# Optimization experiments

Measured on AMD Instinct MI355X. Metric: run time of the kernel, lower is better.

The kernel has to match this reference:

```python
import jax, jax.numpy as jnp
import numpy as np

B, N, D_MODEL, H, D_K, D_V = 4, 1024, 1024, 16, 64, 1024  # N == D_V required by the module's output matmul


def setup_inputs() -> dict:
    key = jax.random.key(0)
    ks = jax.random.split(key, 7)
    def xavier(k, shape):
        fan_in, fan_out = shape[-2], shape[-1]
        std = (2.0 / (fan_in + fan_out)) ** 0.5
        return jax.random.normal(k, shape, dtype=jnp.float32) * std
    return {
        "query": jax.random.normal(ks[0], (B, N, D_MODEL), dtype=jnp.float32),
        "key": jax.random.normal(ks[1], (B, N, D_MODEL), dtype=jnp.float32),
        "value": jax.random.normal(ks[2], (B, N, D_MODEL), dtype=jnp.float32),
        "w_q": xavier(ks[3], (H, D_MODEL, D_K)),
        "w_k": xavier(ks[4], (H, D_MODEL, D_K)),
        "w_v": xavier(ks[5], (H, D_MODEL, D_V)),
        "w_o": xavier(ks[6], (D_MODEL, H * D_V)),
    }


def reference(query, key, value, w_q, w_k, w_v, w_o):
    # Per-head projections: [B,N,d_model] x [H,d_model,d] -> [B,H,N,d]
    q = jnp.einsum('bnd,hdk->bhnk', query, w_q)
    k = jnp.einsum('bnd,hdk->bhnk', key, w_k)
    v = jnp.einsum('bnd,hdv->bhnv', value, w_v)
    scale = 1.0 / jnp.sqrt(jnp.asarray(q.shape[-1], q.dtype))
    scores = jnp.einsum('bhqk,bhmk->bhqm', q, k) * scale  # [B,H,N,N]
    weights = jax.nn.softmax(scores, axis=-1)
    out = jnp.einsum('bhqm,bhmv->bhqv', weights, v)  # [B,H,N,d_v]
    out = out.reshape(out.shape[0], -1, out.shape[-1])  # [B, H*N, d_v]
    # Faithful to source: torch.matmul(w_o, output) with w_o [d_model, H*d_v];
    # requires H*d_v == H*N (N == d_v); result [B, d_model, d_v].
    return jnp.einsum('de,bev->bdv', w_o, out)
```

## Files before the change

### kernel.cpp

```cpp
#include <hip/hip_runtime.h>
#include <hip/hip_bf16.h>

typedef __hip_bfloat16 bf16;
typedef __attribute__((ext_vector_type(8))) short short8;
typedef __attribute__((ext_vector_type(4))) float floatx4;

#define BK 64
#define LDK 72

template<bool OUT_BF16, bool A_F32, bool B_F32>
__global__ void __launch_bounds__(256) gemm_nt(
    const void* __restrict__ Av, const void* __restrict__ Bv, void* __restrict__ Cv,
    int M, int N, int K, int lda, int ldb, int ldc,
    long sA, long sB, long sC)
{
    __shared__ __align__(16) bf16 As[128 * LDK];
    __shared__ __align__(16) bf16 Bs[128 * LDK];

    int bx = blockIdx.x, by = blockIdx.y, bz = blockIdx.z;
    if (gridDim.x == 8 && gridDim.y == 8 && (gridDim.z & 7) == 0) {
        int hw  = bx + (by << 3) + (bz << 6);
        int xcd = hw & 7;
        int idx = hw >> 3;
        int zper = gridDim.z >> 3;
        bz = xcd * zper + (idx >> 6);
        int rem = idx & 63;
        by = rem >> 3;
        bx = rem & 7;
    }

    long aoff = (long)bz * sA;
    long boff = (long)bz * sB;
    long coff = (long)bz * sC;

    int m0 = by * 128;
    int n0 = bx * 128;
    int tid  = threadIdx.x;
    int lane = tid & 63;
    int wave = tid >> 6;
    int quad = lane >> 4;
    int l16  = lane & 15;
    int wm = (wave >> 1) * 64;
    int wn = (wave & 1) * 64;

    int sr = tid >> 3;
    int sc = (tid & 7) * 8;

    floatx4 acc[4][4] = {};

    uint4  pa[4], pb[4];
    float4 pa0[4], pa1[4], pb0[4], pb1[4];

    const int nt = K / BK;

#pragma unroll
    for (int s = 0; s < 4; s++) {
        int r = sr + 32 * s;
        int gm = m0 + r;
        if (A_F32) {
            const float* p = (const float*)Av + aoff + (long)gm * lda + sc;
            if (gm < M) { pa0[s] = *(const float4*)p; pa1[s] = *(const float4*)(p + 4); }
            else { pa0[s] = {0,0,0,0}; pa1[s] = {0,0,0,0}; }
        } else {
            pa[s] = (gm < M) ? *(const uint4*)((const bf16*)Av + aoff + (long)gm * lda + sc)
                             : (uint4){0,0,0,0};
        }
        int gn = n0 + r;
        if (B_F32) {
            const float* p = (const float*)Bv + boff + (long)gn * ldb + sc;
            if (gn < N) { pb0[s] = *(const float4*)p; pb1[s] = *(const float4*)(p + 4); }
            else { pb0[s] = {0,0,0,0}; pb1[s] = {0,0,0,0}; }
        } else {
            pb[s] = (gn < N) ? *(const uint4*)((const bf16*)Bv + boff + (long)gn * ldb + sc)
                             : (uint4){0,0,0,0};
        }
    }

    for (int kt = 0; kt < nt; kt++) {
        __syncthreads();
#pragma unroll
        for (int s = 0; s < 4; s++) {
            int r = sr + 32 * s;
            if (A_F32) {
                bf16 t[8];
                t[0]=__float2bfloat16(pa0[s].x); t[1]=__float2bfloat16(pa0[s].y);
                t[2]=__float2bfloat16(pa0[s].z); t[3]=__float2bfloat16(pa0[s].w);
                t[4]=__float2bfloat16(pa1[s].x); t[5]=__float2bfloat16(pa1[s].y);
                t[6]=__float2bfloat16(pa1[s].z); t[7]=__float2bfloat16(pa1[s].w);
                *(uint4*)(&As[r * LDK + sc]) = *(const uint4*)t;
            } else {
                *(uint4*)(&As[r * LDK + sc]) = pa[s];
            }
            if (B_F32) {
                bf16 t[8];
                t[0]=__float2bfloat16(pb0[s].x); t[1]=__float2bfloat16(pb0[s].y);
                t[2]=__float2bfloat16(pb0[s].z); t[3]=__float2bfloat16(pb0[s].w);
                t[4]=__float2bfloat16(pb1[s].x); t[5]=__float2bfloat16(pb1[s].y);
                t[6]=__float2bfloat16(pb1[s].z); t[7]=__float2bfloat16(pb1[s].w);
                *(uint4*)(&Bs[r * LDK + sc]) = *(const uint4*)t;
            } else {
                *(uint4*)(&Bs[r * LDK + sc]) = pb[s];
            }
        }
        __syncthreads();

        if (kt + 1 < nt) {
            int k0 = (kt + 1) * BK;
#pragma unroll
            for (int s = 0; s < 4; s++) {
                int r = sr + 32 * s;
                int gm = m0 + r;
                if (A_F32) {
                    const float* p = (const float*)Av + aoff + (long)gm * lda + k0 + sc;
                    if (gm < M) { pa0[s] = *(const float4*)p; pa1[s] = *(const float4*)(p + 4); }
                    else { pa0[s] = {0,0,0,0}; pa1[s] = {0,0,0,0}; }
                } else {
                    pa[s] = (gm < M) ? *(const uint4*)((const bf16*)Av + aoff + (long)gm * lda + k0 + sc)
                                     : (uint4){0,0,0,0};
                }
                int gn = n0 + r;
                if (B_F32) {
                    const float* p = (const float*)Bv + boff + (long)gn * ldb + k0 + sc;
                    if (gn < N) { pb0[s] = *(const float4*)p; pb1[s] = *(const float4*)(p + 4); }
                    else { pb0[s] = {0,0,0,0}; pb1[s] = {0,0,0,0}; }
                } else {
                    pb[s] = (gn < N) ? *(const uint4*)((const bf16*)Bv + boff + (long)gn * ldb + k0 + sc)
                                     : (uint4){0,0,0,0};
                }
            }
        }

#pragma unroll
        for (int ks = 0; ks < 2; ks++) {
            short8 af[4], bfr[4];
#pragma unroll
            for (int i = 0; i < 4; i++)
                af[i] = *(const short8*)(&As[(wm + i * 16 + l16) * LDK + ks * 32 + quad * 8]);
#pragma unroll
            for (int j = 0; j < 4; j++)
                bfr[j] = *(const short8*)(&Bs[(wn + j * 16 + l16) * LDK + ks * 32 + quad * 8]);
#pragma unroll
            for (int i = 0; i < 4; i++)
#pragma unroll
                for (int j = 0; j < 4; j++)
                    acc[i][j] = __builtin_amdgcn_mfma_f32_16x16x32_bf16(af[i], bfr[j], acc[i][j], 0, 0, 0);
        }
    }

#pragma unroll
    for (int i = 0; i < 4; i++) {
        int row = m0 + wm + i * 16 + quad * 4;
#pragma unroll
        for (int j = 0; j < 4; j++) {
            int col = n0 + wn + j * 16 + l16;
            if (col >= N) continue;
#pragma unroll
            for (int v = 0; v < 4; v++) {
                int r = row + v;
                if (r < M) {
                    float val = acc[i][j][v];
                    if (OUT_BF16)
                        ((bf16*)Cv)[coff + (long)r * ldc + col] = __float2bfloat16(val);
                    else
                        ((float*)Cv)[coff + (long)r * ldc + col] = val;
                }
            }
        }
    }
}

__global__ void __launch_bounds__(256) attn_softmax(
    const bf16* __restrict__ Q, const bf16* __restrict__ Kb, bf16* __restrict__ Wts)
{
    __shared__ __align__(16) bf16 Ks[64 * 72];

    int h = blockIdx.y;
    const bf16* Qbh = Q  + (long)h * 262144;
    const bf16* Kbh = Kb + (long)h * 262144;
    bf16* W = Wts + (long)h * 1048576;

    int tid  = threadIdx.x;
    int lane = tid & 63;
    int wave = tid >> 6;
    int quad = lane >> 4;
    int l16  = lane & 15;
    int q0 = blockIdx.x * 64 + wave * 16;

    short8 a0 = *(const short8*)(Qbh + (long)(q0 + l16) * 64 + quad * 8);
    short8 a1 = *(const short8*)(Qbh + (long)(q0 + l16) * 64 + 32 + quad * 8);

    int sr = tid >> 3;
    int sc = (tid & 7) * 8;

    const float scale = 0.125f;
    float m_v[4] = {-1e30f, -1e30f, -1e30f, -1e30f};
    float l_v[4] = {0.f, 0.f, 0.f, 0.f};

    for (int t = 0; t < 16; t++) {
        __syncthreads();
        const bf16* src = Kbh + (long)(t * 64 + sr) * 64 + sc;
        *(uint4*)(&Ks[sr * 72 + sc])        = *(const uint4*)src;
        *(uint4*)(&Ks[(sr + 32) * 72 + sc]) = *(const uint4*)(src + 32 * 64);
        __syncthreads();
#pragma unroll
        for (int j = 0; j < 4; j++) {
            short8 b0 = *(const short8*)(&Ks[(j * 16 + l16) * 72 + quad * 8]);
            short8 b1 = *(const short8*)(&Ks[(j * 16 + l16) * 72 + 32 + quad * 8]);
            floatx4 acc = {0.f, 0.f, 0.f, 0.f};
            acc = __builtin_amdgcn_mfma_f32_16x16x32_bf16(a0, b0, acc, 0, 0, 0);
            acc = __builtin_amdgcn_mfma_f32_16x16x32_bf16(a1, b1, acc, 0, 0, 0);
#pragma unroll
            for (int v = 0; v < 4; v++) {
                float s  = acc[v] * scale;
                float nm = fmaxf(m_v[v], s);
                l_v[v] = l_v[v] * __expf(m_v[v] - nm) + __expf(s - nm);
                m_v[v] = nm;
            }
        }
    }

#pragma unroll
    for (int d = 1; d < 16; d <<= 1) {
#pragma unroll
        for (int v = 0; v < 4; v++) {
            float om = __shfl_xor(m_v[v], d);
            float ol = __shfl_xor(l_v[v], d);
            float nm = fmaxf(m_v[v], om);
            l_v[v] = l_v[v] * __expf(m_v[v] - nm) + ol * __expf(om - nm);
            m_v[v] = nm;
        }
    }
    float linv[4];
#pragma unroll
    for (int v = 0; v < 4; v++) linv[v] = 1.0f / l_v[v];

    for (int t = 0; t < 16; t++) {
        __syncthreads();
        const bf16* src = Kbh + (long)(t * 64 + sr) * 64 + sc;
        *(uint4*)(&Ks[sr * 72 + sc])        = *(const uint4*)src;
        *(uint4*)(&Ks[(sr + 32) * 72 + sc]) = *(const uint4*)(src + 32 * 64);
        __syncthreads();
#pragma unroll
        for (int j = 0; j < 4; j++) {
            short8 b0 = *(const short8*)(&Ks[(j * 16 + l16) * 72 + quad * 8]);
            short8 b1 = *(const short8*)(&Ks[(j * 16 + l16) * 72 + 32 + quad * 8]);
            floatx4 acc = {0.f, 0.f, 0.f, 0.f};
            acc = __builtin_amdgcn_mfma_f32_16x16x32_bf16(a0, b0, acc, 0, 0, 0);
            acc = __builtin_amdgcn_mfma_f32_16x16x32_bf16(a1, b1, acc, 0, 0, 0);
#pragma unroll
            for (int v = 0; v < 4; v++) {
                float w = __expf(acc[v] * scale - m_v[v]) * linv[v];
                W[(long)(q0 + quad * 4 + v) * 1024 + t * 64 + j * 16 + l16] = __float2bfloat16(w);
            }
        }
    }
}

__global__ void __launch_bounds__(256) cast_bf16_k(
    const float* __restrict__ in, bf16* __restrict__ out, int n4)
{
    int i = blockIdx.x * 256 + threadIdx.x;
    if (i >= n4) return;
    float4 v = ((const float4*)in)[i];
    bf16 t[4] = {__float2bfloat16(v.x), __float2bfloat16(v.y),
                 __float2bfloat16(v.z), __float2bfloat16(v.w)};
    ((uint2*)out)[i] = *(const uint2*)t;
}

__global__ void __launch_bounds__(256) transpose_cast(
    const float* __restrict__ in, bf16* __restrict__ out, int R, int C)
{
    __shared__ float t[32][33];
    int h = blockIdx.z;
    const float* inh = in + (long)h * R * C;
    bf16* outh = out + (long)h * R * C;
    int c0 = blockIdx.x * 32, r0 = blockIdx.y * 32;
    int tx = threadIdx.x, ty = threadIdx.y;
#pragma unroll
    for (int i = 0; i < 32; i += 8)
        t[ty + i][tx] = inh[(long)(r0 + ty + i) * C + c0 + tx];
    __syncthreads();
#pragma unroll
    for (int i = 0; i < 32; i += 8)
        outh[(long)(c0 + ty + i) * R + r0 + tx] = __float2bfloat16(t[tx][ty + i]);
}

__global__ void __launch_bounds__(256) reduce16_k(
    const float* __restrict__ part, float* __restrict__ out)
{
    int i = blockIdx.x * 256 + threadIdx.x;
    float4 s = ((const float4*)part)[i];
#pragma unroll
    for (int c = 1; c < 16; c++) {
        float4 p = ((const float4*)part)[c * 262144 + i];
        s.x += p.x; s.y += p.y; s.z += p.z; s.w += p.w;
    }
    ((float4*)out)[i] = s;
}

extern "C" void kernel_launch(void* const* d_in, const int* in_sizes, int n_in,
                              void* d_out, int out_size, void* d_ws, size_t ws_size,
                              hipStream_t stream) {
    const float* query = (const float*)d_in[0];
    const float* key   = (const float*)d_in[1];
    const float* value = (const float*)d_in[2];
    const float* w_q   = (const float*)d_in[3];
    const float* w_k   = (const float*)d_in[4];
    const float* w_v   = (const float*)d_in[5];
    const float* w_o   = (const float*)d_in[6];
    float* out = (float*)d_out;

    char* ws = (char*)d_ws;
    const size_t MB = (size_t)1 << 20;
    bf16* wqt      = (bf16*)(ws + 0 * MB);
    bf16* wkt      = (bf16*)(ws + 2 * MB);
    bf16* wvt      = (bf16*)(ws + 4 * MB);
    bf16* wob      = (bf16*)(ws + 36 * MB);
    bf16* qb       = (bf16*)(ws + 68 * MB);
    bf16* kb       = (bf16*)(ws + 76 * MB);
    bf16* vt_b     = (bf16*)(ws + 84 * MB);
    bf16* wts_b    = (bf16*)(ws + 116 * MB);
    bf16* att_b    = (bf16*)(ws + 148 * MB);
    float* out_part = (float*)(ws + 84 * MB);

    transpose_cast<<<dim3(2, 32, 16),  dim3(32, 8), 0, stream>>>(w_q, wqt, 1024, 64);
    transpose_cast<<<dim3(2, 32, 16),  dim3(32, 8), 0, stream>>>(w_k, wkt, 1024, 64);
    transpose_cast<<<dim3(32, 32, 16), dim3(32, 8), 0, stream>>>(w_v, wvt, 1024, 1024);
    cast_bf16_k<<<16384, 256, 0, stream>>>(w_o, wob, 1024 * 16384 / 4);

    gemm_nt<true, true, false><<<dim3(1, 32, 16), 256, 0, stream>>>(
        query, wqt, qb, 4096, 64, 1024, 1024, 1024, 64, 0L, 65536L, 262144L);
    gemm_nt<true, true, false><<<dim3(1, 32, 16), 256, 0, stream>>>(
        key, wkt, kb, 4096, 64, 1024, 1024, 1024, 64, 0L, 65536L, 262144L);

    for (int b = 0; b < 4; b++) {
        gemm_nt<true, false, true><<<dim3(8, 8, 16), 256, 0, stream>>>(
            wvt, value + (long)b * 1048576, vt_b,
            1024, 1024, 1024, 1024, 1024, 1024, 1048576L, 0L, 1048576L);

        attn_softmax<<<dim3(16, 16), 256, 0, stream>>>(
            qb + (long)b * 65536, kb + (long)b * 65536, wts_b);

        gemm_nt<true, false, false><<<dim3(8, 8, 16), 256, 0, stream>>>(
            vt_b, wts_b, att_b,
            1024, 1024, 1024, 1024, 1024, 16384, 1048576L, 1048576L, 1024L);

        gemm_nt<false, false, false><<<dim3(8, 8, 16), 256, 0, stream>>>(
            wob, att_b, out_part,
            1024, 1024, 1024, 16384, 16384, 1024, 1024L, 1024L, 1048576L);

        reduce16_k<<<1024, 256, 0, stream>>>(out_part, out + (long)b * 1048576);
    }

    (void)in_sizes; (void)n_in; (void)out_size; (void)ws_size;
}
```

Measured before the change: 1.022 ms.

## Add direct global-to-LDS bf16 GEMM with XOR swizzle for the big matmuls

Adds a new bf16-only NT GEMM kernel that uses global_load_lds to copy 16-byte chunks straight into shared memory with an XOR-swizzled layout, skipping register staging and padding. The value tensor is pre-cast to bf16 per batch so the V projection can use this path, and the three large per-batch GEMMs switch to the new kernel. This is meant to cut load instruction count and LDS bank conflicts. It adds an extra cast kernel per batch and has no double buffering, and value_bf shares workspace with att_b, which is safe only because the V projection finishes before att_b is written.

```diff
diff --git a/kernel.cpp b/kernel.cpp
--- a/kernel.cpp
+++ b/kernel.cpp
@@ -7,6 +7,108 @@
 
 #define BK 64
 #define LDK 72
+
+__device__ __forceinline__ void gload_lds16(const void* g, void* l) {
+    __builtin_amdgcn_global_load_lds(
+        (const __attribute__((address_space(1))) void*)g,
+        (__attribute__((address_space(3))) void*)l, 16, 0, 0);
+}
+
+template<bool OUT_BF16>
+__global__ void __launch_bounds__(256) gemm_nt_lds(
+    const bf16* __restrict__ A, const bf16* __restrict__ B, void* __restrict__ Cv,
+    int M, int N, int K, int lda, int ldb, int ldc,
+    long sA, long sB, long sC)
+{
+    __shared__ __align__(16) bf16 As[128 * 64];
+    __shared__ __align__(16) bf16 Bs[128 * 64];
+
+    int bx = blockIdx.x, by = blockIdx.y, bz = blockIdx.z;
+    if (gridDim.x == 8 && gridDim.y == 8 && (gridDim.z & 7) == 0) {
+        int hw  = bx + (by << 3) + (bz << 6);
+        int xcd = hw & 7;
+        int idx = hw >> 3;
+        int zper = gridDim.z >> 3;
+        bz = xcd * zper + (idx >> 6);
+        int rem = idx & 63;
+        by = rem >> 3;
+        bx = rem & 7;
+    }
+
+    long aoff = (long)bz * sA;
+    long boff = (long)bz * sB;
+    long coff = (long)bz * sC;
+
+    int m0 = by * 128;
+    int n0 = bx * 128;
+    int tid  = threadIdx.x;
+    int lane = tid & 63;
+    int wave = tid >> 6;
+    int quad = lane >> 4;
+    int l16  = lane & 15;
+    int wm = (wave >> 1) * 64;
+    int wn = (wave & 1) * 64;
+
+    int lrow   = lane >> 3;
+    int lchunk = (lane & 7) ^ lrow;
+    int swz    = l16 & 7;
+
+    const bf16* Abase = A + aoff + (long)m0 * lda;
+    const bf16* Bbase = B + boff + (long)n0 * ldb;
+
+    floatx4 acc[4][4] = {};
+    const int nt = K / BK;
+
+    for (int kt = 0; kt < nt; kt++) {
+        __syncthreads();
+        long kofs = (long)kt * BK;
+#pragma unroll
+        for (int s = 0; s < 4; s++) {
+            int r = wave * 32 + s * 8;
+            gload_lds16(Abase + (long)(r + lrow) * lda + kofs + lchunk * 8, &As[r * 64]);
+            gload_lds16(Bbase + (long)(r + lrow) * ldb + kofs + lchunk * 8, &Bs[r * 64]);
+        }
+        __syncthreads();
+
+#pragma unroll
+        for (int ks = 0; ks < 2; ks++) {
+            short8 af[4], bfr[4];
+#pragma unroll
+            for (int i = 0; i < 4; i++) {
+                int ri = wm + i * 16 + l16;
+                af[i] = *(const short8*)(&As[ri * 64 + (((ks << 2) | quad) ^ swz) * 8]);
+            }
+#pragma unroll
+            for (int j = 0; j < 4; j++) {
+                int rj = wn + j * 16 + l16;
+                bfr[j] = *(const short8*)(&Bs[rj * 64 + (((ks << 2) | quad) ^ swz) * 8]);
+            }
+#pragma unroll
+            for (int i = 0; i < 4; i++)
+#pragma unroll
+                for (int j = 0; j < 4; j++)
+                    acc[i][j] = __builtin_amdgcn_mfma_f32_16x16x32_bf16(af[i], bfr[j], acc[i][j], 0, 0, 0);
+        }
+    }
+
+#pragma unroll
+    for (int i = 0; i < 4; i++) {
+        int row = m0 + wm + i * 16 + quad * 4;
+#pragma unroll
+        for (int j = 0; j < 4; j++) {
+            int col = n0 + wn + j * 16 + l16;
+#pragma unroll
+            for (int v = 0; v < 4; v++) {
+                int r = row + v;
+                float val = acc[i][j][v];
+                if (OUT_BF16)
+                    ((bf16*)Cv)[coff + (long)r * ldc + col] = __float2bfloat16(val);
+                else
+                    ((float*)Cv)[coff + (long)r * ldc + col] = val;
+            }
+        }
+    }
+}
 
 template<bool OUT_BF16, bool A_F32, bool B_F32>
 __global__ void __launch_bounds__(256) gemm_nt(
@@ -321,6 +423,7 @@
     bf16* vt_b     = (bf16*)(ws + 84 * MB);
     bf16* wts_b    = (bf16*)(ws + 116 * MB);
     bf16* att_b    = (bf16*)(ws + 148 * MB);
+    bf16* value_bf = (bf16*)(ws + 148 * MB);
     float* out_part = (float*)(ws + 84 * MB);
 
     transpose_cast<<<dim3(2, 32, 16),  dim3(32, 8), 0, stream>>>(w_q, wqt, 1024, 64);
@@ -334,18 +437,20 @@
         key, wkt, kb, 4096, 64, 1024, 1024, 1024, 64, 0L, 65536L, 262144L);
 
     for (int b = 0; b < 4; b++) {
-        gemm_nt<true, false, true><<<dim3(8, 8, 16), 256, 0, stream>>>(
-            wvt, value + (long)b * 1048576, vt_b,
+        cast_bf16_k<<<1024, 256, 0, stream>>>(value + (long)b * 1048576, value_bf, 262144);
+
+        gemm_nt_lds<true><<<dim3(8, 8, 16), 256, 0, stream>>>(
+            wvt, value_bf, vt_b,
             1024, 1024, 1024, 1024, 1024, 1024, 1048576L, 0L, 1048576L);
 
         attn_softmax<<<dim3(16, 16), 256, 0, stream>>>(
             qb + (long)b * 65536, kb + (long)b * 65536, wts_b);
 
-        gemm_nt<true, false, false><<<dim3(8, 8, 16), 256, 0, stream>>>(
+        gemm_nt_lds<true><<<dim3(8, 8, 16), 256, 0, stream>>>(
             vt_b, wts_b, att_b,
             1024, 1024, 1024, 1024, 1024, 16384, 1048576L, 1048576L, 1024L);
 
-        gemm_nt<false, false, false><<<dim3(8, 8, 16), 256, 0, stream>>>(
+        gemm_nt_lds<false><<<dim3(8, 8, 16), 256, 0, stream>>>(
             wob, att_b, out_part,
             1024, 1024, 1024, 16384, 16384, 1024, 1024L, 1024L, 1048576L);
 
```

New measurement: 1.016 ms. No clear change (-0.6%).
